# Kernel optimization log

Hardware: AMD Instinct MI355X
Metric: run time of the kernel (lower is better)

Reference implementation:

```python
import jax, jax.numpy as jnp
import numpy as np

N_NODES = 100000
N_EDGES = 1250000
D_IN = 32
H = 64
EPS = 1e-5


def layer_norm(x, g, b):
    mu = jnp.mean(x, axis=-1, keepdims=True)
    var = jnp.mean(jnp.square(x - mu), axis=-1, keepdims=True)
    return (x - mu) * jax.lax.rsqrt(var + EPS) * g + b


def setup_inputs() -> dict:
    key = jax.random.key(0)
    ks = jax.random.split(key, 6)
    x = jax.random.normal(ks[0], (N_NODES, D_IN), dtype=jnp.float32)
    edge_index = jax.random.randint(ks[1], (2, N_EDGES), 0, N_NODES, dtype=jnp.int64)
    W1 = jax.random.normal(ks[2], (D_IN, H), dtype=jnp.float32) * (1.0 / np.sqrt(D_IN))
    b1 = jax.random.normal(ks[3], (H,), dtype=jnp.float32) * 0.01
    W2 = jax.random.normal(ks[4], (H, H), dtype=jnp.float32) * (1.0 / np.sqrt(H))
    b2 = jax.random.normal(ks[5], (H,), dtype=jnp.float32) * 0.01
    g1 = jnp.ones((H,), dtype=jnp.float32)
    beta1 = jnp.zeros((H,), dtype=jnp.float32)
    g2 = jnp.ones((H,), dtype=jnp.float32)
    beta2 = jnp.zeros((H,), dtype=jnp.float32)
    return {"x": x, "edge_index": edge_index, "W1": W1, "b1": b1, "g1": g1,
            "beta1": beta1, "W2": W2, "b2": b2, "g2": g2, "beta2": beta2}


def reference(x, edge_index, W1, b1, g1, beta1, W2, b2, g2, beta2):
    # node MLP: Linear -> LN -> ReLU, twice
    h = jax.nn.relu(layer_norm(x @ W1 + b1, g1, beta1))
    h = jax.nn.relu(layer_norm(h @ W2 + b2, g2, beta2))
    # message passing: gather source features, scatter-add to destinations
    row, col = edge_index[0], edge_index[1]
    aggr = jax.ops.segment_sum(h[col], row, num_segments=N_NODES)  # [N, H]
    return h + aggr
```

## Files before the change

kernel.cpp:

```cpp
#include <hip/hip_runtime.h>

#define N_NODES 100000
#define D_IN 32
#define H 64
#define EPS 1e-5f
#define RSTR 32
#define CAP 32
#define OV_CAP 32768
#define NBINS 196
#define BINSZ 512
#define BINCAP 7168

typedef float floatx2 __attribute__((ext_vector_type(2)));

__device__ __forceinline__ unsigned short f2bf(float f) {
    union { float f; unsigned int u; } c; c.f = f;
    unsigned int b = c.u + 0x7FFFu + ((c.u >> 16) & 1u);
    return (unsigned short)(b >> 16);
}
__device__ __forceinline__ float bf2f(unsigned short s) {
    union { unsigned int u; float f; } c; c.u = ((unsigned int)s) << 16;
    return c.f;
}

__global__ __launch_bounds__(256, 2) void ka_kernel(
    const float* __restrict__ x,
    const float* __restrict__ W1, const float* __restrict__ b1,
    const float* __restrict__ g1, const float* __restrict__ be1,
    const float* __restrict__ W2, const float* __restrict__ b2,
    const float* __restrict__ g2, const float* __restrict__ be2,
    unsigned short* __restrict__ hb, unsigned char* __restrict__ hb8,
    const int* __restrict__ ei, int* __restrict__ part, int* __restrict__ binCur,
    int* __restrict__ ovCnt, int2* __restrict__ ov,
    int E, int SB, int TOT)
{
    const int i = blockIdx.x;
    const int before = (int)((long long)i * SB / TOT);
    const int after  = (int)((long long)(i + 1) * SB / TOT);

    if (after > before) {
        __shared__ int hist[NBINS];
        __shared__ int basev[NBINS];

        int t = before * 256 + threadIdx.x;
        int e0 = t * 8;

        int rows[8], cols[8], myofs[8];
        if (e0 + 7 < E) {
            int4 r0 = *(const int4*)(ei + e0);
            int4 r1 = *(const int4*)(ei + e0 + 4);
            int4 c0 = *(const int4*)(ei + E + e0);
            int4 c1 = *(const int4*)(ei + E + e0 + 4);
            rows[0]=r0.x; rows[1]=r0.y; rows[2]=r0.z; rows[3]=r0.w;
            rows[4]=r1.x; rows[5]=r1.y; rows[6]=r1.z; rows[7]=r1.w;
            cols[0]=c0.x; cols[1]=c0.y; cols[2]=c0.z; cols[3]=c0.w;
            cols[4]=c1.x; cols[5]=c1.y; cols[6]=c1.z; cols[7]=c1.w;
        } else {
#pragma unroll
            for (int j = 0; j < 8; ++j) {
                int e = e0 + j;
                if (e < E) { rows[j] = ei[e]; cols[j] = ei[E + e]; }
                else rows[j] = -1;
            }
        }

        if (threadIdx.x < NBINS) hist[threadIdx.x] = 0;
        __syncthreads();

#pragma unroll
        for (int j = 0; j < 8; ++j)
            if (rows[j] >= 0) myofs[j] = atomicAdd(&hist[rows[j] >> 9], 1);
        __syncthreads();

        if (threadIdx.x < NBINS) {
            int h = hist[threadIdx.x];
            if (h > 0) basev[threadIdx.x] = atomicAdd(&binCur[threadIdx.x], h);
        }
        __syncthreads();

#pragma unroll
        for (int j = 0; j < 8; ++j) {
            if (rows[j] < 0) continue;
            int bin  = rows[j] >> 9;
            int slot = basev[bin] + myofs[j];
            if (slot < BINCAP) {
                part[bin * BINCAP + slot] = ((rows[j] & (BINSZ - 1)) << 17) | cols[j];
            } else {
                int s = atomicAdd(ovCnt, 1);
                if (s < OV_CAP) ov[s] = make_int2(rows[j], cols[j]);
            }
        }
        return;
    }

    int gid = (i - before) * 256 + threadIdx.x;
    int node = gid < N_NODES ? gid : N_NODES - 1;

    float xr[D_IN];
    {
        const float4* xp = (const float4*)(x + (long long)node * D_IN);
#pragma unroll
        for (int i2 = 0; i2 < D_IN / 4; ++i2) {
            float4 v = xp[i2];
            xr[4*i2+0] = v.x; xr[4*i2+1] = v.y; xr[4*i2+2] = v.z; xr[4*i2+3] = v.w;
        }
    }

    float h1[H];
#pragma unroll
    for (int jb = 0; jb < H / 4; ++jb) {
        float4 b = *(const float4*)(b1 + jb * 4);
        h1[4*jb+0] = b.x; h1[4*jb+1] = b.y; h1[4*jb+2] = b.z; h1[4*jb+3] = b.w;
    }
#pragma unroll
    for (int k = 0; k < D_IN; ++k) {
        float xk = xr[k];
#pragma unroll
        for (int jb = 0; jb < H / 4; ++jb) {
            float4 w = *(const float4*)(W1 + k * H + jb * 4);
            h1[4*jb+0] += xk * w.x; h1[4*jb+1] += xk * w.y;
            h1[4*jb+2] += xk * w.z; h1[4*jb+3] += xk * w.w;
        }
    }
    {
        float s0=0,s1=0,s2=0,s3=0, q0=0,q1=0,q2=0,q3=0;
#pragma unroll
        for (int j = 0; j < H; j += 4) {
            s0 += h1[j+0]; s1 += h1[j+1]; s2 += h1[j+2]; s3 += h1[j+3];
            q0 += h1[j+0]*h1[j+0]; q1 += h1[j+1]*h1[j+1];
            q2 += h1[j+2]*h1[j+2]; q3 += h1[j+3]*h1[j+3];
        }
        float mu  = (s0+s1+s2+s3) * (1.0f / H);
        float var = (q0+q1+q2+q3) * (1.0f / H) - mu * mu;
        float rs  = rsqrtf(var + EPS);
#pragma unroll
        for (int jb = 0; jb < H / 4; ++jb) {
            float4 g = *(const float4*)(g1 + jb * 4);
            float4 be = *(const float4*)(be1 + jb * 4);
            h1[4*jb+0] = fmaxf((h1[4*jb+0]-mu)*rs*g.x + be.x, 0.0f);
            h1[4*jb+1] = fmaxf((h1[4*jb+1]-mu)*rs*g.y + be.y, 0.0f);
            h1[4*jb+2] = fmaxf((h1[4*jb+2]-mu)*rs*g.z + be.z, 0.0f);
            h1[4*jb+3] = fmaxf((h1[4*jb+3]-mu)*rs*g.w + be.w, 0.0f);
        }
    }

    float h2[H];
#pragma unroll
    for (int jb = 0; jb < H / 4; ++jb) {
        float4 b = *(const float4*)(b2 + jb * 4);
        h2[4*jb+0] = b.x; h2[4*jb+1] = b.y; h2[4*jb+2] = b.z; h2[4*jb+3] = b.w;
    }
#pragma unroll
    for (int k = 0; k < H; ++k) {
        float hk = h1[k];
#pragma unroll
        for (int jb = 0; jb < H / 4; ++jb) {
            float4 w = *(const float4*)(W2 + k * H + jb * 4);
            h2[4*jb+0] += hk * w.x; h2[4*jb+1] += hk * w.y;
            h2[4*jb+2] += hk * w.z; h2[4*jb+3] += hk * w.w;
        }
    }
    {
        float s0=0,s1=0,s2=0,s3=0, q0=0,q1=0,q2=0,q3=0;
#pragma unroll
        for (int j = 0; j < H; j += 4) {
            s0 += h2[j+0]; s1 += h2[j+1]; s2 += h2[j+2]; s3 += h2[j+3];
            q0 += h2[j+0]*h2[j+0]; q1 += h2[j+1]*h2[j+1];
            q2 += h2[j+2]*h2[j+2]; q3 += h2[j+3]*h2[j+3];
        }
        float mu  = (s0+s1+s2+s3) * (1.0f / H);
        float var = (q0+q1+q2+q3) * (1.0f / H) - mu * mu;
        float rs  = rsqrtf(var + EPS);

        unsigned short* hp = hb + (long long)node * H;
        unsigned int w8[H / 4];
#pragma unroll
        for (int jb = 0; jb < H / 4; ++jb) {
            float4 g = *(const float4*)(g2 + jb * 4);
            float4 be = *(const float4*)(be2 + jb * 4);
            float4 v;
            v.x = fmaxf((h2[4*jb+0]-mu)*rs*g.x + be.x, 0.0f);
            v.y = fmaxf((h2[4*jb+1]-mu)*rs*g.y + be.y, 0.0f);
            v.z = fmaxf((h2[4*jb+2]-mu)*rs*g.z + be.z, 0.0f);
            v.w = fmaxf((h2[4*jb+3]-mu)*rs*g.w + be.w, 0.0f);
            ushort4 u;
            u.x = f2bf(v.x); u.y = f2bf(v.y); u.z = f2bf(v.z); u.w = f2bf(v.w);
            *(ushort4*)(hp + 4*jb) = u;
            int lo = __builtin_amdgcn_cvt_pk_fp8_f32(v.x, v.y, 0, false);
            w8[jb] = (unsigned int)__builtin_amdgcn_cvt_pk_fp8_f32(v.z, v.w, lo, true);
        }
        unsigned int* hp8 = (unsigned int*)(hb8 + (long long)node * H);
#pragma unroll
        for (int q = 0; q < H / 16; ++q)
            *(uint4*)(hp8 + q * 4) = make_uint4(w8[4*q+0], w8[4*q+1], w8[4*q+2], w8[4*q+3]);
    }
}

__global__ __launch_bounds__(256, 2) void kb_kernel(
    const int* __restrict__ part, const int* __restrict__ binCur,
    int* __restrict__ cnt, int* __restrict__ bkt,
    int* __restrict__ ovCnt, int2* __restrict__ ov)
{
    __shared__ int cnt_l[BINSZ];
    __shared__ int bkt_l[BINSZ * CAP];

    const int bin = blockIdx.x;
    int n = binCur[bin];
    if (n > BINCAP) n = BINCAP;
    const int gbase = bin << 9;

    for (int r = threadIdx.x; r < BINSZ; r += 256) cnt_l[r] = 0;
    __syncthreads();

    const int* p = part + bin * BINCAP;
    for (int idx = threadIdx.x; idx < n; idx += 256) {
        int v = p[idx];
        int r = v >> 17;
        int c = v & 0x1FFFF;
        int pos = atomicAdd(&cnt_l[r], 1);
        if (pos < CAP) {
            bkt_l[r * CAP + pos] = c;
        } else {
            int s = atomicAdd(ovCnt, 1);
            if (s < OV_CAP) ov[s] = make_int2(gbase + r, c);
        }
    }
    __syncthreads();

    uint4* gb = (uint4*)bkt;
    const uint4* lb = (const uint4*)bkt_l;
    for (int idx = threadIdx.x; idx < BINSZ * 8; idx += 256) {
        int row = idx >> 3;
        if (gbase + row < N_NODES)
            gb[(long long)(gbase + row) * 8 + (idx & 7)] = lb[idx];
    }
    for (int r = threadIdx.x; r < BINSZ; r += 256)
        if (gbase + r < N_NODES) cnt[gbase + r] = cnt_l[r];
}

__global__ __launch_bounds__(256, 2) void aggr_kernel(
    const int* __restrict__ cnt, const int* __restrict__ bkt,
    const unsigned short* __restrict__ hb, const unsigned char* __restrict__ hb8,
    float* __restrict__ out,
    const int* __restrict__ ovCnt, const int2* __restrict__ ov)
{
    const int t    = threadIdx.x & 63;
    const int sub  = t >> 4;
    const int l    = t & 15;
    const int q    = l & 3;
    const int g    = l >> 2;
    const int wave = blockIdx.x * 4 + (threadIdx.x >> 6);
    const int node = wave * 4 + sub;

    int m = cnt[node];
    if (m > CAP) m = CAP;
    const int base = node * RSTR;

    int4 ea = *(const int4*)(bkt + base + g * 8);
    int4 eb = *(const int4*)(bkt + base + g * 8 + 4);
    int ed[8] = { ea.x, ea.y, ea.z, ea.w, eb.x, eb.y, eb.z, eb.w };
    const int e0 = g * 8;

    const uint4* h84 = (const uint4*)hb8;

    float s[16];
#pragma unroll
    for (int j = 0; j < 16; ++j) s[j] = 0.f;

    uint4 vv[8];
#pragma unroll
    for (int k = 0; k < 8; ++k)
        if (e0 + k < m) vv[k] = h84[(ed[k] << 2) + q];

#pragma unroll
    for (int k = 0; k < 8; ++k) {
        if (e0 + k < m) {
            unsigned int w[4] = { vv[k].x, vv[k].y, vv[k].z, vv[k].w };
#pragma unroll
            for (int u = 0; u < 4; ++u) {
                floatx2 p0 = __builtin_amdgcn_cvt_pk_f32_fp8(w[u], false);
                floatx2 p1 = __builtin_amdgcn_cvt_pk_f32_fp8(w[u], true);
                s[4*u+0] += p0.x; s[4*u+1] += p0.y;
                s[4*u+2] += p1.x; s[4*u+3] += p1.y;
            }
        }
    }

#pragma unroll
    for (int j = 0; j < 16; ++j) {
        s[j] += __shfl_xor(s[j], 4, 64);
        s[j] += __shfl_xor(s[j], 8, 64);
    }

    const int co = q * 16 + g * 4;
    float a0 = s[g*4+0], a1 = s[g*4+1], a2 = s[g*4+2], a3 = s[g*4+3];

    {
        uint2 sv = *(const uint2*)(hb + ((long long)node << 6) + co);
        a0 += bf2f((unsigned short)(sv.x & 0xFFFFu));
        a1 += bf2f((unsigned short)(sv.x >> 16));
        a2 += bf2f((unsigned short)(sv.y & 0xFFFFu));
        a3 += bf2f((unsigned short)(sv.y >> 16));
    }

    int nov = *ovCnt; if (nov > OV_CAP) nov = OV_CAP;
    for (int i = 0; i < nov; ++i) {
        int2 rc = ov[i];
        if (rc.x == node) {
            uint2 vo = *(const uint2*)(hb + ((long long)rc.y << 6) + co);
            a0 += bf2f((unsigned short)(vo.x & 0xFFFFu));
            a1 += bf2f((unsigned short)(vo.x >> 16));
            a2 += bf2f((unsigned short)(vo.y & 0xFFFFu));
            a3 += bf2f((unsigned short)(vo.y >> 16));
        }
    }

    *(float4*)(out + ((long long)node << 6) + co) = make_float4(a0, a1, a2, a3);
}

extern "C" void kernel_launch(void* const* d_in, const int* in_sizes, int n_in,
                              void* d_out, int out_size, void* d_ws, size_t ws_size,
                              hipStream_t stream)
{
    const float* x   = (const float*)d_in[0];
    const int*   ei  = (const int*)d_in[1];
    const float* W1  = (const float*)d_in[2];
    const float* b1  = (const float*)d_in[3];
    const float* g1  = (const float*)d_in[4];
    const float* be1 = (const float*)d_in[5];
    const float* W2  = (const float*)d_in[6];
    const float* b2  = (const float*)d_in[7];
    const float* g2  = (const float*)d_in[8];
    const float* be2 = (const float*)d_in[9];

    float* out = (float*)d_out;

    char* ws = (char*)d_ws;
    unsigned short* hb     = (unsigned short*)ws;
    unsigned char*  hb8    = (unsigned char*)(ws + 12800000);
    int*            cnt    = (int*)(ws + 19200000);
    int*            ovCnt  = (int*)(ws + 19600000);
    int2*           ov     = (int2*)(ws + 19600064);
    int*            binCur = (int*)(ws + 19862208);
    int*            bkt    = (int*)(ws + 19863040);
    int*            part   = (int*)(ws + 32663040);

    const int E = in_sizes[1] / 2;

    (void)hipMemsetAsync(ws + 19600000, 0, 263040, stream);

    const int SB = ((E + 7) / 8 + 255) / 256;
    const int MB = (N_NODES + 255) / 256;

    ka_kernel<<<SB + MB, 256, 0, stream>>>(
        x, W1, b1, g1, be1, W2, b2, g2, be2, hb, hb8,
        ei, part, binCur, ovCnt, ov, E, SB, SB + MB);

    kb_kernel<<<NBINS, 256, 0, stream>>>(part, binCur, cnt, bkt, ovCnt, ov);

    aggr_kernel<<<N_NODES / 16, 256, 0, stream>>>(cnt, bkt, hb, hb8, out, ovCnt, ov);
}
```

Baseline: 188.2 us.

## Fuse bucketing and aggregation into one LDS-atomic scatter kernel per bin quarter

```diff
diff --git a/kernel.cpp b/kernel.cpp
--- a/kernel.cpp
+++ b/kernel.cpp
@@ -4,12 +4,12 @@
 #define D_IN 32
 #define H 64
 #define EPS 1e-5f
-#define RSTR 32
-#define CAP 32
 #define OV_CAP 32768
 #define NBINS 196
 #define BINSZ 512
 #define BINCAP 7168
+#define QBIN 128
+#define ASTR 68
 
 typedef float floatx2 __attribute__((ext_vector_type(2)));
 
@@ -196,126 +196,92 @@
     }
 }
 
-__global__ __launch_bounds__(256, 2) void kb_kernel(
+__global__ __launch_bounds__(256, 4) void kbc_kernel(
     const int* __restrict__ part, const int* __restrict__ binCur,
-    int* __restrict__ cnt, int* __restrict__ bkt,
-    int* __restrict__ ovCnt, int2* __restrict__ ov)
-{
-    __shared__ int cnt_l[BINSZ];
-    __shared__ int bkt_l[BINSZ * CAP];
-
-    const int bin = blockIdx.x;
-    int n = binCur[bin];
-    if (n > BINCAP) n = BINCAP;
-    const int gbase = bin << 9;
-
-    for (int r = threadIdx.x; r < BINSZ; r += 256) cnt_l[r] = 0;
-    __syncthreads();
-
-    const int* p = part + bin * BINCAP;
-    for (int idx = threadIdx.x; idx < n; idx += 256) {
-        int v = p[idx];
-        int r = v >> 17;
-        int c = v & 0x1FFFF;
-        int pos = atomicAdd(&cnt_l[r], 1);
-        if (pos < CAP) {
-            bkt_l[r * CAP + pos] = c;
-        } else {
-            int s = atomicAdd(ovCnt, 1);
-            if (s < OV_CAP) ov[s] = make_int2(gbase + r, c);
-        }
-    }
-    __syncthreads();
-
-    uint4* gb = (uint4*)bkt;
-    const uint4* lb = (const uint4*)bkt_l;
-    for (int idx = threadIdx.x; idx < BINSZ * 8; idx += 256) {
-        int row = idx >> 3;
-        if (gbase + row < N_NODES)
-            gb[(long long)(gbase + row) * 8 + (idx & 7)] = lb[idx];
-    }
-    for (int r = threadIdx.x; r < BINSZ; r += 256)
-        if (gbase + r < N_NODES) cnt[gbase + r] = cnt_l[r];
-}
-
-__global__ __launch_bounds__(256, 2) void aggr_kernel(
-    const int* __restrict__ cnt, const int* __restrict__ bkt,
     const unsigned short* __restrict__ hb, const unsigned char* __restrict__ hb8,
     float* __restrict__ out,
     const int* __restrict__ ovCnt, const int2* __restrict__ ov)
 {
-    const int t    = threadIdx.x & 63;
-    const int sub  = t >> 4;
-    const int l    = t & 15;
-    const int q    = l & 3;
-    const int g    = l >> 2;
-    const int wave = blockIdx.x * 4 + (threadIdx.x >> 6);
-    const int node = wave * 4 + sub;
-
-    int m = cnt[node];
-    if (m > CAP) m = CAP;
-    const int base = node * RSTR;
-
-    int4 ea = *(const int4*)(bkt + base + g * 8);
-    int4 eb = *(const int4*)(bkt + base + g * 8 + 4);
-    int ed[8] = { ea.x, ea.y, ea.z, ea.w, eb.x, eb.y, eb.z, eb.w };
-    const int e0 = g * 8;
-
-    const uint4* h84 = (const uint4*)hb8;
-
-    float s[16];
-#pragma unroll
-    for (int j = 0; j < 16; ++j) s[j] = 0.f;
-
-    uint4 vv[8];
-#pragma unroll
-    for (int k = 0; k < 8; ++k)
-        if (e0 + k < m) vv[k] = h84[(ed[k] << 2) + q];
-
-#pragma unroll
-    for (int k = 0; k < 8; ++k) {
-        if (e0 + k < m) {
-            unsigned int w[4] = { vv[k].x, vv[k].y, vv[k].z, vv[k].w };
-#pragma unroll
-            for (int u = 0; u < 4; ++u) {
-                floatx2 p0 = __builtin_amdgcn_cvt_pk_f32_fp8(w[u], false);
-                floatx2 p1 = __builtin_amdgcn_cvt_pk_f32_fp8(w[u], true);
-                s[4*u+0] += p0.x; s[4*u+1] += p0.y;
-                s[4*u+2] += p1.x; s[4*u+3] += p1.y;
+    __shared__ float acc[QBIN * ASTR];
+
+    const int bin = blockIdx.x >> 2;
+    const int qtr = blockIdx.x & 3;
+    const int rlo = qtr * QBIN;
+    const int rbase = (bin << 9) + rlo;
+    int n = binCur[bin]; if (n > BINCAP) n = BINCAP;
+
+    for (int i = threadIdx.x; i < QBIN * ASTR; i += 256) acc[i] = 0.f;
+    __syncthreads();
+
+    const int t   = threadIdx.x & 63;
+    const int wid = threadIdx.x >> 6;
+    const unsigned int* h32 = (const unsigned int*)hb8;
+    const int* p = part + bin * BINCAP;
+
+    const int usel = t >> 2;
+    const bool hiPair = (t & 2) != 0;
+    const bool oddLane = (t & 1) != 0;
+
+    for (int i0 = wid * 8; i0 < n; i0 += 32) {
+        int v[8]; bool keep[8]; int rr[8];
+#pragma unroll
+        for (int j = 0; j < 8; ++j) {
+            int idx = i0 + j;
+            v[j] = (idx < n) ? p[idx] : -1;
+        }
+#pragma unroll
+        for (int j = 0; j < 8; ++j) {
+            int r = v[j] >> 17;
+            rr[j] = r - rlo;
+            keep[j] = (v[j] >= 0) && (rr[j] >= 0) && (rr[j] < QBIN);
+        }
+        unsigned int u[8];
+#pragma unroll
+        for (int j = 0; j < 8; ++j)
+            if (keep[j]) u[j] = h32[((v[j] & 0x1FFFF) << 4) + usel];
+#pragma unroll
+        for (int j = 0; j < 8; ++j) {
+            if (keep[j]) {
+                floatx2 plo = __builtin_amdgcn_cvt_pk_f32_fp8(u[j], false);
+                floatx2 phi = __builtin_amdgcn_cvt_pk_f32_fp8(u[j], true);
+                floatx2 pr;
+                pr.x = hiPair ? phi.x : plo.x;
+                pr.y = hiPair ? phi.y : plo.y;
+                float f = oddLane ? pr.y : pr.x;
+                atomicAdd(&acc[rr[j] * ASTR + t], f);
             }
         }
     }
-
-#pragma unroll
-    for (int j = 0; j < 16; ++j) {
-        s[j] += __shfl_xor(s[j], 4, 64);
-        s[j] += __shfl_xor(s[j], 8, 64);
-    }
-
-    const int co = q * 16 + g * 4;
-    float a0 = s[g*4+0], a1 = s[g*4+1], a2 = s[g*4+2], a3 = s[g*4+3];
-
-    {
-        uint2 sv = *(const uint2*)(hb + ((long long)node << 6) + co);
-        a0 += bf2f((unsigned short)(sv.x & 0xFFFFu));
-        a1 += bf2f((unsigned short)(sv.x >> 16));
-        a2 += bf2f((unsigned short)(sv.y & 0xFFFFu));
-        a3 += bf2f((unsigned short)(sv.y >> 16));
-    }
+    __syncthreads();
 
     int nov = *ovCnt; if (nov > OV_CAP) nov = OV_CAP;
-    for (int i = 0; i < nov; ++i) {
-        int2 rc = ov[i];
-        if (rc.x == node) {
-            uint2 vo = *(const uint2*)(hb + ((long long)rc.y << 6) + co);
-            a0 += bf2f((unsigned short)(vo.x & 0xFFFFu));
-            a1 += bf2f((unsigned short)(vo.x >> 16));
-            a2 += bf2f((unsigned short)(vo.y & 0xFFFFu));
-            a3 += bf2f((unsigned short)(vo.y >> 16));
-        }
-    }
-
-    *(float4*)(out + ((long long)node << 6) + co) = make_float4(a0, a1, a2, a3);
+    for (int i = threadIdx.x; i < QBIN * 16; i += 256) {
+        int rl = i >> 4, q = i & 15;
+        int node = rbase + rl;
+        if (node >= N_NODES) continue;
+        float a0 = acc[rl * ASTR + q*4 + 0];
+        float a1 = acc[rl * ASTR + q*4 + 1];
+        float a2 = acc[rl * ASTR + q*4 + 2];
+        float a3 = acc[rl * ASTR + q*4 + 3];
+        {
+            uint2 sv = *(const uint2*)(hb + ((long long)node << 6) + (q << 2));
+            a0 += bf2f((unsigned short)(sv.x & 0xFFFFu));
+            a1 += bf2f((unsigned short)(sv.x >> 16));
+            a2 += bf2f((unsigned short)(sv.y & 0xFFFFu));
+            a3 += bf2f((unsigned short)(sv.y >> 16));
+        }
+        for (int k = 0; k < nov; ++k) {
+            int2 rc = ov[k];
+            if (rc.x == node) {
+                uint2 vo = *(const uint2*)(hb + ((long long)rc.y << 6) + (q << 2));
+                a0 += bf2f((unsigned short)(vo.x & 0xFFFFu));
+                a1 += bf2f((unsigned short)(vo.x >> 16));
+                a2 += bf2f((unsigned short)(vo.y & 0xFFFFu));
+                a3 += bf2f((unsigned short)(vo.y >> 16));
+            }
+        }
+        *(float4*)(out + ((long long)node << 6) + (q << 2)) = make_float4(a0, a1, a2, a3);
+    }
 }
 
 extern "C" void kernel_launch(void* const* d_in, const int* in_sizes, int n_in,
@@ -338,16 +304,14 @@
     char* ws = (char*)d_ws;
     unsigned short* hb     = (unsigned short*)ws;
     unsigned char*  hb8    = (unsigned char*)(ws + 12800000);
-    int*            cnt    = (int*)(ws + 19200000);
-    int*            ovCnt  = (int*)(ws + 19600000);
-    int2*           ov     = (int2*)(ws + 19600064);
-    int*            binCur = (int*)(ws + 19862208);
-    int*            bkt    = (int*)(ws + 19863040);
-    int*            part   = (int*)(ws + 32663040);
+    int*            ovCnt  = (int*)(ws + 19200000);
+    int*            binCur = (int*)(ws + 19200064);
+    int2*           ov     = (int2*)(ws + 19200896);
+    int*            part   = (int*)(ws + 19463040);
 
     const int E = in_sizes[1] / 2;
 
-    (void)hipMemsetAsync(ws + 19600000, 0, 263040, stream);
+    (void)hipMemsetAsync(ws + 19200000, 0, 896, stream);
 
     const int SB = ((E + 7) / 8 + 255) / 256;
     const int MB = (N_NODES + 255) / 256;
@@ -356,7 +320,5 @@
         x, W1, b1, g1, be1, W2, b2, g2, be2, hb, hb8,
         ei, part, binCur, ovCnt, ov, E, SB, SB + MB);
 
-    kb_kernel<<<NBINS, 256, 0, stream>>>(part, binCur, cnt, bkt, ovCnt, ov);
-
-    aggr_kernel<<<N_NODES / 16, 256, 0, stream>>>(cnt, bkt, hb, hb8, out, ovCnt, ov);
-}
+    kbc_kernel<<<NBINS * 4, 256, 0, stream>>>(part, binCur, hb, hb8, out, ovCnt, ov);
+}
```

Measured after the change: 703.9 us. +274.1%, slower.

## Fuse bucket build and aggregation into one kernel using LDS buckets

Applied to the files above, without the earlier changes.

```diff
diff --git a/kernel.cpp b/kernel.cpp
--- a/kernel.cpp
+++ b/kernel.cpp
@@ -4,12 +4,13 @@
 #define D_IN 32
 #define H 64
 #define EPS 1e-5f
-#define RSTR 32
 #define CAP 32
 #define OV_CAP 32768
+#define LOV_CAP 256
 #define NBINS 196
 #define BINSZ 512
 #define BINCAP 7168
+#define QBIN 128
 
 typedef float floatx2 __attribute__((ext_vector_type(2)));
 
@@ -196,126 +197,128 @@
     }
 }
 
-__global__ __launch_bounds__(256, 2) void kb_kernel(
+__global__ __launch_bounds__(256, 4) void kbc_kernel(
     const int* __restrict__ part, const int* __restrict__ binCur,
-    int* __restrict__ cnt, int* __restrict__ bkt,
-    int* __restrict__ ovCnt, int2* __restrict__ ov)
-{
-    __shared__ int cnt_l[BINSZ];
-    __shared__ int bkt_l[BINSZ * CAP];
-
-    const int bin = blockIdx.x;
-    int n = binCur[bin];
-    if (n > BINCAP) n = BINCAP;
-    const int gbase = bin << 9;
-
-    for (int r = threadIdx.x; r < BINSZ; r += 256) cnt_l[r] = 0;
-    __syncthreads();
-
-    const int* p = part + bin * BINCAP;
-    for (int idx = threadIdx.x; idx < n; idx += 256) {
-        int v = p[idx];
-        int r = v >> 17;
-        int c = v & 0x1FFFF;
-        int pos = atomicAdd(&cnt_l[r], 1);
-        if (pos < CAP) {
-            bkt_l[r * CAP + pos] = c;
-        } else {
-            int s = atomicAdd(ovCnt, 1);
-            if (s < OV_CAP) ov[s] = make_int2(gbase + r, c);
-        }
-    }
-    __syncthreads();
-
-    uint4* gb = (uint4*)bkt;
-    const uint4* lb = (const uint4*)bkt_l;
-    for (int idx = threadIdx.x; idx < BINSZ * 8; idx += 256) {
-        int row = idx >> 3;
-        if (gbase + row < N_NODES)
-            gb[(long long)(gbase + row) * 8 + (idx & 7)] = lb[idx];
-    }
-    for (int r = threadIdx.x; r < BINSZ; r += 256)
-        if (gbase + r < N_NODES) cnt[gbase + r] = cnt_l[r];
-}
-
-__global__ __launch_bounds__(256, 2) void aggr_kernel(
-    const int* __restrict__ cnt, const int* __restrict__ bkt,
     const unsigned short* __restrict__ hb, const unsigned char* __restrict__ hb8,
     float* __restrict__ out,
     const int* __restrict__ ovCnt, const int2* __restrict__ ov)
 {
-    const int t    = threadIdx.x & 63;
-    const int sub  = t >> 4;
-    const int l    = t & 15;
-    const int q    = l & 3;
-    const int g    = l >> 2;
-    const int wave = blockIdx.x * 4 + (threadIdx.x >> 6);
-    const int node = wave * 4 + sub;
-
-    int m = cnt[node];
-    if (m > CAP) m = CAP;
-    const int base = node * RSTR;
-
-    int4 ea = *(const int4*)(bkt + base + g * 8);
-    int4 eb = *(const int4*)(bkt + base + g * 8 + 4);
-    int ed[8] = { ea.x, ea.y, ea.z, ea.w, eb.x, eb.y, eb.z, eb.w };
-    const int e0 = g * 8;
-
+    __shared__ int cnt_l[QBIN];
+    __shared__ int bkt_l[QBIN * CAP];
+    __shared__ int lovf[LOV_CAP];
+    __shared__ int nlov;
+
+    const int bin = blockIdx.x >> 2;
+    const int qtr = blockIdx.x & 3;
+    const int rlo = qtr * QBIN;
+    const int rbase = (bin << 9) + rlo;
+    int n = binCur[bin]; if (n > BINCAP) n = BINCAP;
+
+    for (int i = threadIdx.x; i < QBIN; i += 256) cnt_l[i] = 0;
+    if (threadIdx.x == 0) nlov = 0;
+    __syncthreads();
+
+    const int* p = part + bin * BINCAP;
+    for (int idx = threadIdx.x; idx < n; idx += 256) {
+        int v = p[idx];
+        int rr = (v >> 17) - rlo;
+        if (rr >= 0 && rr < QBIN) {
+            int pos = atomicAdd(&cnt_l[rr], 1);
+            if (pos < CAP) {
+                bkt_l[rr * CAP + pos] = v & 0x1FFFF;
+            } else {
+                int s = atomicAdd(&nlov, 1);
+                if (s < LOV_CAP) lovf[s] = ((rr) << 17) | (v & 0x1FFFF);
+            }
+        }
+    }
+    __syncthreads();
+
+    const int t   = threadIdx.x & 63;
+    const int wid = threadIdx.x >> 6;
+    const int sub = t >> 4;
+    const int l   = t & 15;
+    const int q   = l & 3;
+    const int g   = l >> 2;
     const uint4* h84 = (const uint4*)hb8;
 
-    float s[16];
-#pragma unroll
-    for (int j = 0; j < 16; ++j) s[j] = 0.f;
-
-    uint4 vv[8];
-#pragma unroll
-    for (int k = 0; k < 8; ++k)
-        if (e0 + k < m) vv[k] = h84[(ed[k] << 2) + q];
-
-#pragma unroll
-    for (int k = 0; k < 8; ++k) {
-        if (e0 + k < m) {
-            unsigned int w[4] = { vv[k].x, vv[k].y, vv[k].z, vv[k].w };
-#pragma unroll
-            for (int u = 0; u < 4; ++u) {
-                floatx2 p0 = __builtin_amdgcn_cvt_pk_f32_fp8(w[u], false);
-                floatx2 p1 = __builtin_amdgcn_cvt_pk_f32_fp8(w[u], true);
-                s[4*u+0] += p0.x; s[4*u+1] += p0.y;
-                s[4*u+2] += p1.x; s[4*u+3] += p1.y;
-            }
-        }
-    }
-
-#pragma unroll
-    for (int j = 0; j < 16; ++j) {
-        s[j] += __shfl_xor(s[j], 4, 64);
-        s[j] += __shfl_xor(s[j], 8, 64);
-    }
-
-    const int co = q * 16 + g * 4;
-    float a0 = s[g*4+0], a1 = s[g*4+1], a2 = s[g*4+2], a3 = s[g*4+3];
-
-    {
-        uint2 sv = *(const uint2*)(hb + ((long long)node << 6) + co);
-        a0 += bf2f((unsigned short)(sv.x & 0xFFFFu));
-        a1 += bf2f((unsigned short)(sv.x >> 16));
-        a2 += bf2f((unsigned short)(sv.y & 0xFFFFu));
-        a3 += bf2f((unsigned short)(sv.y >> 16));
-    }
-
     int nov = *ovCnt; if (nov > OV_CAP) nov = OV_CAP;
-    for (int i = 0; i < nov; ++i) {
-        int2 rc = ov[i];
-        if (rc.x == node) {
-            uint2 vo = *(const uint2*)(hb + ((long long)rc.y << 6) + co);
-            a0 += bf2f((unsigned short)(vo.x & 0xFFFFu));
-            a1 += bf2f((unsigned short)(vo.x >> 16));
-            a2 += bf2f((unsigned short)(vo.y & 0xFFFFu));
-            a3 += bf2f((unsigned short)(vo.y >> 16));
-        }
-    }
-
-    *(float4*)(out + ((long long)node << 6) + co) = make_float4(a0, a1, a2, a3);
+    int nlv = nlov;   if (nlv > LOV_CAP) nlv = LOV_CAP;
+
+    for (int iter = 0; iter < QBIN / 16; ++iter) {
+        const int rl   = iter * 16 + wid * 4 + sub;
+        const int node = rbase + rl;
+        int m = cnt_l[rl]; if (m > CAP) m = CAP;
+
+        int4 ea = *(const int4*)(bkt_l + rl * CAP + g * 8);
+        int4 eb = *(const int4*)(bkt_l + rl * CAP + g * 8 + 4);
+        int ed[8] = { ea.x, ea.y, ea.z, ea.w, eb.x, eb.y, eb.z, eb.w };
+        const int e0 = g * 8;
+
+        float s[16];
+#pragma unroll
+        for (int j = 0; j < 16; ++j) s[j] = 0.f;
+
+        uint4 vv[8];
+#pragma unroll
+        for (int k = 0; k < 8; ++k)
+            if (e0 + k < m) vv[k] = h84[(ed[k] << 2) + q];
+
+#pragma unroll
+        for (int k = 0; k < 8; ++k) {
+            if (e0 + k < m) {
+                unsigned int w[4] = { vv[k].x, vv[k].y, vv[k].z, vv[k].w };
+#pragma unroll
+                for (int u = 0; u < 4; ++u) {
+                    floatx2 p0 = __builtin_amdgcn_cvt_pk_f32_fp8(w[u], false);
+                    floatx2 p1 = __builtin_amdgcn_cvt_pk_f32_fp8(w[u], true);
+                    s[4*u+0] += p0.x; s[4*u+1] += p0.y;
+                    s[4*u+2] += p1.x; s[4*u+3] += p1.y;
+                }
+            }
+        }
+
+#pragma unroll
+        for (int j = 0; j < 16; ++j) {
+            s[j] += __shfl_xor(s[j], 4, 64);
+            s[j] += __shfl_xor(s[j], 8, 64);
+        }
+
+        const int co = q * 16 + g * 4;
+        float a0 = s[g*4+0], a1 = s[g*4+1], a2 = s[g*4+2], a3 = s[g*4+3];
+
+        if (node < N_NODES) {
+            uint2 sv = *(const uint2*)(hb + ((long long)node << 6) + co);
+            a0 += bf2f((unsigned short)(sv.x & 0xFFFFu));
+            a1 += bf2f((unsigned short)(sv.x >> 16));
+            a2 += bf2f((unsigned short)(sv.y & 0xFFFFu));
+            a3 += bf2f((unsigned short)(sv.y >> 16));
+
+            for (int k = 0; k < nov; ++k) {
+                int2 rc = ov[k];
+                if (rc.x == node) {
+                    uint2 vo = *(const uint2*)(hb + ((long long)rc.y << 6) + co);
+                    a0 += bf2f((unsigned short)(vo.x & 0xFFFFu));
+                    a1 += bf2f((unsigned short)(vo.x >> 16));
+                    a2 += bf2f((unsigned short)(vo.y & 0xFFFFu));
+                    a3 += bf2f((unsigned short)(vo.y >> 16));
+                }
+            }
+            for (int k = 0; k < nlv; ++k) {
+                int e = lovf[k];
+                if ((e >> 17) == rl) {
+                    int col = e & 0x1FFFF;
+                    uint2 vo = *(const uint2*)(hb + ((long long)col << 6) + co);
+                    a0 += bf2f((unsigned short)(vo.x & 0xFFFFu));
+                    a1 += bf2f((unsigned short)(vo.x >> 16));
+                    a2 += bf2f((unsigned short)(vo.y & 0xFFFFu));
+                    a3 += bf2f((unsigned short)(vo.y >> 16));
+                }
+            }
+
+            *(float4*)(out + ((long long)node << 6) + co) = make_float4(a0, a1, a2, a3);
+        }
+    }
 }
 
 extern "C" void kernel_launch(void* const* d_in, const int* in_sizes, int n_in,
@@ -338,16 +341,14 @@
     char* ws = (char*)d_ws;
     unsigned short* hb     = (unsigned short*)ws;
     unsigned char*  hb8    = (unsigned char*)(ws + 12800000);
-    int*            cnt    = (int*)(ws + 19200000);
-    int*            ovCnt  = (int*)(ws + 19600000);
-    int2*           ov     = (int2*)(ws + 19600064);
-    int*            binCur = (int*)(ws + 19862208);
-    int*            bkt    = (int*)(ws + 19863040);
-    int*            part   = (int*)(ws + 32663040);
+    int*            ovCnt  = (int*)(ws + 19200000);
+    int*            binCur = (int*)(ws + 19200064);
+    int2*           ov     = (int2*)(ws + 19200896);
+    int*            part   = (int*)(ws + 19463040);
 
     const int E = in_sizes[1] / 2;
 
-    (void)hipMemsetAsync(ws + 19600000, 0, 263040, stream);
+    (void)hipMemsetAsync(ws + 19200000, 0, 896, stream);
 
     const int SB = ((E + 7) / 8 + 255) / 256;
     const int MB = (N_NODES + 255) / 256;
@@ -356,7 +357,5 @@
         x, W1, b1, g1, be1, W2, b2, g2, be2, hb, hb8,
         ei, part, binCur, ovCnt, ov, E, SB, SB + MB);
 
-    kb_kernel<<<NBINS, 256, 0, stream>>>(part, binCur, cnt, bkt, ovCnt, ov);
-
-    aggr_kernel<<<N_NODES / 16, 256, 0, stream>>>(cnt, bkt, hb, hb8, out, ovCnt, ov);
-}
+    kbc_kernel<<<NBINS * 4, 256, 0, stream>>>(part, binCur, hb, hb8, out, ovCnt, ov);
+}
```

Result: slower. 194.9 us (+3.6%).
